# Kernel tuning notes

Hardware: AMD Instinct MI355X
Metric: run time of the kernel (lower is better)

Reference implementation:

```python
import jax, jax.numpy as jnp
import numpy as np

M = 100        # n_models
D = 16         # input_dim
H = 128        # hidden_dim
O = 1          # output_dim
NH = 4         # n_hidden
N = 16384      # batch of query points


def setup_inputs() -> dict:
    key = jax.random.key(0)
    ks = jax.random.split(key, 9)
    s = 0.1
    return {
        "x": jax.random.normal(ks[0], (N, D), dtype=jnp.float32),
        "W1": jax.random.normal(ks[1], (M, H, D), dtype=jnp.float32) * s,
        "b1": jax.random.normal(ks[2], (M, H), dtype=jnp.float32) * s,
        "Wh": jax.random.normal(ks[3], (M, NH, H, H), dtype=jnp.float32) * s,
        "bh": jax.random.normal(ks[4], (M, NH, H), dtype=jnp.float32) * s,
        "Wmu": jax.random.normal(ks[5], (M, O, H), dtype=jnp.float32) * s,
        "bmu": jax.random.normal(ks[6], (M, O), dtype=jnp.float32) * s,
        "Wsig": jax.random.normal(ks[7], (M, O, H), dtype=jnp.float32) * s,
        "bsig": jax.random.normal(ks[8], (M, O), dtype=jnp.float32) * s,
    }


def reference(x, W1, b1, Wh, bh, Wmu, bmu, Wsig, bsig):
    # Batched across all M models: h has shape [M, N, H]
    h = jax.nn.relu(jnp.einsum("nd,mhd->mnh", x, W1) + b1[:, None, :])
    for i in range(NH):  # fixed small structural loop over hidden layers
        h = jax.nn.relu(jnp.einsum("mnh,mkh->mnk", h, Wh[:, i]) + bh[:, i][:, None, :])
    mu = jnp.einsum("mnh,moh->mno", h, Wmu) + bmu[:, None, :]      # [M, N, O]
    sigma = jnp.exp(jnp.einsum("mnh,moh->mno", h, Wsig) + bsig[:, None, :])
    return (mu, sigma)
```

## Files before the change

kernel.cpp:

```cpp
#include <hip/hip_runtime.h>


typedef float  f32x4  __attribute__((ext_vector_type(4)));
typedef float  f32x16 __attribute__((ext_vector_type(16)));
typedef __bf16 bf16x4 __attribute__((ext_vector_type(4)));
typedef __bf16 bf16x8 __attribute__((ext_vector_type(8)));
typedef short  s16x4  __attribute__((ext_vector_type(4)));

union BF4  { bf16x4 v; uint2 u2; };
union FRAG { bf16x8 v; uint4 u4; };
union PKW  { uint2 u2; s16x4 s4; };

#define MODELS 100
#define NPT    16384
#define HDIM   128
#define SG_OFF (MODELS * NPT)

#define XB_OFF   0
#define W1B_OFF  262144
#define WHB_OFF  466944
#define WMU_OFF  7020544
#define WSG_OFF  7033344

#define GTOT 880768

__global__ __launch_bounds__(256) void cvt_weights(
    const float* __restrict__ x,   const float* __restrict__ W1,
    const float* __restrict__ Wh,  const float* __restrict__ Wmu,
    const float* __restrict__ Wsg, unsigned short* __restrict__ ws)
{
  int gid = blockIdx.x * 256 + threadIdx.x;
  if (gid >= GTOT) return;
  const float* src;
  unsigned int dst;
  if (gid < 32768) {
    src = x + gid * 8;                       dst = XB_OFF + gid * 8;
  } else if (gid < 58368) {
    int g = gid - 32768;
    src = W1 + g * 8;                        dst = W1B_OFF + g * 8;
  } else if (gid < 877568) {
    int g = gid - 58368;
    int chunk  = g >> 11;
    int within = g & 2047;
    int r   = within >> 4;
    int j   = within & 15;
    src = Wh + (size_t)g * 8;
    dst = WHB_OFF + chunk * 16384 + (j * 128 + r) * 8;
  } else if (gid < 879168) {
    int g = gid - 877568;
    src = Wmu + g * 8;                       dst = WMU_OFF + g * 8;
  } else {
    int g = gid - 879168;
    src = Wsg + g * 8;                       dst = WSG_OFF + g * 8;
  }
  f32x4 a = *(const f32x4*)src;
  f32x4 b = *(const f32x4*)(src + 4);
  BF4 lo, hi;
  lo.v = __builtin_convertvector(a, bf16x4);
  hi.v = __builtin_convertvector(b, bf16x4);
  uint4 u; u.x = lo.u2.x; u.y = lo.u2.y; u.z = hi.u2.x; u.w = hi.u2.y;
  *(uint4*)&ws[dst] = u;
}

__device__ __forceinline__ void gload_lds16(const void* g, void* l) {
  __builtin_amdgcn_global_load_lds(
      (const __attribute__((address_space(1))) void*)g,
      (__attribute__((address_space(3))) void*)l, 16, 0, 0);
}

#define MFMA32(A,B,C) __builtin_amdgcn_mfma_f32_32x32x16_bf16((A),(B),(C),0,0,0)

__device__ __forceinline__ void build_hfrag(const f32x16 (&acc)[2][4],
                                            uint4 (&hf)[2][8]) {
  const s16x4 z4 = {0, 0, 0, 0};
  #pragma unroll
  for (int nt = 0; nt < 2; ++nt) {
    #pragma unroll
    for (int kt2 = 0; kt2 < 4; ++kt2) {
      uint2 P[4];
      #pragma unroll
      for (int q = 0; q < 4; ++q) {
        f32x4 v;
        v[0] = acc[nt][kt2][4*q+0]; v[1] = acc[nt][kt2][4*q+1];
        v[2] = acc[nt][kt2][4*q+2]; v[3] = acc[nt][kt2][4*q+3];
        BF4 b; b.v = __builtin_convertvector(v, bf16x4);
        PKW p; p.u2 = b.u2;
        p.s4 = __builtin_elementwise_max(p.s4, z4);
        P[q] = p.u2;
      }
      #pragma unroll
      for (int sb = 0; sb < 2; ++sb) {
        unsigned int x0 = P[2*sb].x, y0 = P[2*sb+1].x;
        unsigned int x1 = P[2*sb].y, y1 = P[2*sb+1].y;
        asm("v_permlane32_swap_b32 %0, %1" : "+v"(x0), "+v"(y0));
        asm("v_permlane32_swap_b32 %0, %1" : "+v"(x1), "+v"(y1));
        uint4 f; f.x = x0; f.y = x1; f.z = y0; f.w = y1;
        hf[nt][2*kt2+sb] = f;
      }
    }
  }
}

__global__ __launch_bounds__(512, 2) void ens_mlp(
    const unsigned short* __restrict__ ws,
    const float* __restrict__ b1,  const float* __restrict__ bh,
    const float* __restrict__ bmu, const float* __restrict__ bsg,
    float* __restrict__ out)
{
  __shared__ unsigned short wlds[4 * HDIM * HDIM];

  const int bid = blockIdx.x;
  const int swz = (bid & 7) * 400 + (bid >> 3);
  const int m   = swz >> 5;
  const int nb0 = (swz & 31) << 9;

  const int t    = threadIdx.x;
  const int lane = t & 63;
  const int wv   = t >> 6;
  const int l31  = lane & 31;
  const int hi   = lane >> 5;
  const int nbw  = nb0 + wv * 64;

  {
    const char* src = (const char*)(ws + WHB_OFF + m * 65536);
    char* dst = (char*)wlds;
    #pragma unroll
    for (int it = 0; it < 16; ++it) {
      int off = t * 16 + it * 8192;
      gload_lds16(src + off, dst + off);
    }
  }

  uint4  hfrag[2][8];
  f32x16 acc[2][4];

  auto layer1 = [&]() {
    const unsigned short* W1m = ws + W1B_OFF + m * (HDIM * 16);
    const unsigned short* xp  = ws + XB_OFF;
    FRAG w1f[4], xf[2];
    #pragma unroll
    for (int kt2 = 0; kt2 < 4; ++kt2)
      w1f[kt2].v = *(const bf16x8*)&W1m[(kt2 * 32 + l31) * 16 + hi * 8];
    #pragma unroll
    for (int nt = 0; nt < 2; ++nt)
      xf[nt].v = *(const bf16x8*)&xp[(nbw + nt * 32 + l31) * 16 + hi * 8];
    #pragma unroll
    for (int kt2 = 0; kt2 < 4; ++kt2) {
      union { f32x16 v; f32x4 q[4]; } C;
      #pragma unroll
      for (int q = 0; q < 4; ++q)
        C.q[q] = *(const f32x4*)(b1 + m * HDIM + kt2 * 32 + q * 8 + hi * 4);
      #pragma unroll
      for (int nt = 0; nt < 2; ++nt)
        acc[nt][kt2] = MFMA32(w1f[kt2].v, xf[nt].v, C.v);
    }
    build_hfrag(acc, hfrag);
  };

  if (wv < 4) layer1();
  __syncthreads();
  if (wv >= 4) layer1();

  #pragma unroll
  for (int i = 0; i < 4; ++i) {
    const unsigned short* wl = wlds + i * 16384 + l31 * 8 + hi * 1024;
    const float* bp = bh + m * 512 + i * HDIM;

    union { f32x16 v; f32x4 q[4]; } C[4];
    #pragma unroll
    for (int kt2 = 0; kt2 < 4; ++kt2)
      #pragma unroll
      for (int q = 0; q < 4; ++q)
        C[kt2].q[q] = *(const f32x4*)(bp + kt2 * 32 + q * 8 + hi * 4);

    #pragma unroll
    for (int ks = 0; ks < 8; ++ks) {
      FRAG wf[4];
      #pragma unroll
      for (int kt2 = 0; kt2 < 4; ++kt2)
        wf[kt2].u4 = *(const uint4*)(wl + kt2 * 256 + ks * 2048);
      #pragma unroll
      for (int kt2 = 0; kt2 < 4; ++kt2)
        #pragma unroll
        for (int nt = 0; nt < 2; ++nt) {
          FRAG hv; hv.u4 = hfrag[nt][ks];
          acc[nt][kt2] = MFMA32(wf[kt2].v, hv.v,
                                ks == 0 ? C[kt2].v : acc[nt][kt2]);
        }
    }
    build_hfrag(acc, hfrag);
  }

  {
    FRAG hw[8];
    const unsigned short* wp = ws + (l31 == 0 ? WMU_OFF : WSG_OFF) + m * HDIM;
    #pragma unroll
    for (int ks = 0; ks < 8; ++ks) {
      if (l31 < 2) {
        hw[ks].v = *(const bf16x8*)&wp[ks * 16 + hi * 8];
      } else {
        uint4 z; z.x = 0u; z.y = 0u; z.z = 0u; z.w = 0u;
        hw[ks].u4 = z;
      }
    }
    f32x16 C;
    #pragma unroll
    for (int j = 0; j < 16; ++j) C[j] = 0.0f;
    if (hi == 0) { C[0] = bmu[m]; C[1] = bsg[m]; }

    #pragma unroll
    for (int nt = 0; nt < 2; ++nt) {
      f32x16 a2;
      #pragma unroll
      for (int ks = 0; ks < 8; ++ks) {
        FRAG hv; hv.u4 = hfrag[nt][ks];
        a2 = MFMA32(hw[ks].v, hv.v, ks == 0 ? C : a2);
      }
      if (hi == 0) {
        int n = nbw + nt * 32 + l31;
        out[m * NPT + n]          = a2[0];
        out[SG_OFF + m * NPT + n] = expf(a2[1]);
      }
    }
  }
}

extern "C" void kernel_launch(void* const* d_in, const int* in_sizes, int n_in,
                              void* d_out, int out_size, void* d_ws, size_t ws_size,
                              hipStream_t stream) {
  const float* x   = (const float*)d_in[0];
  const float* W1  = (const float*)d_in[1];
  const float* b1  = (const float*)d_in[2];
  const float* Wh  = (const float*)d_in[3];
  const float* bh  = (const float*)d_in[4];
  const float* Wmu = (const float*)d_in[5];
  const float* bmu = (const float*)d_in[6];
  const float* Wsg = (const float*)d_in[7];
  const float* bsg = (const float*)d_in[8];
  unsigned short* ws = (unsigned short*)d_ws;
  (void)in_sizes; (void)n_in; (void)out_size; (void)ws_size;

  cvt_weights<<<(GTOT + 255) / 256, 256, 0, stream>>>(x, W1, Wh, Wmu, Wsg, ws);
  ens_mlp<<<3200, 512, 0, stream>>>(ws, b1, bh, bmu, bsg, (float*)d_out);
}
```

Before: 225.1 us.

## Ping-pong two point tiles so activation conversion overlaps MFMA work

```diff
diff --git a/kernel.cpp b/kernel.cpp
--- a/kernel.cpp
+++ b/kernel.cpp
@@ -7,9 +7,7 @@
 typedef __bf16 bf16x8 __attribute__((ext_vector_type(8)));
 typedef short  s16x4  __attribute__((ext_vector_type(4)));
 
-union BF4  { bf16x4 v; uint2 u2; };
-union FRAG { bf16x8 v; uint4 u4; };
-union PKW  { uint2 u2; s16x4 s4; };
+union BF4 { bf16x4 v; uint2 u2; };
 
 #define MODELS 100
 #define NPT    16384
@@ -70,34 +68,27 @@
 
 #define MFMA32(A,B,C) __builtin_amdgcn_mfma_f32_32x32x16_bf16((A),(B),(C),0,0,0)
 
-__device__ __forceinline__ void build_hfrag(const f32x16 (&acc)[2][4],
-                                            uint4 (&hf)[2][8]) {
+__device__ __forceinline__ void build_chunk(const f32x16& a, bf16x8 (&hf)[8],
+                                            int base) {
   const s16x4 z4 = {0, 0, 0, 0};
-  #pragma unroll
-  for (int nt = 0; nt < 2; ++nt) {
-    #pragma unroll
-    for (int kt2 = 0; kt2 < 4; ++kt2) {
-      uint2 P[4];
-      #pragma unroll
-      for (int q = 0; q < 4; ++q) {
-        f32x4 v;
-        v[0] = acc[nt][kt2][4*q+0]; v[1] = acc[nt][kt2][4*q+1];
-        v[2] = acc[nt][kt2][4*q+2]; v[3] = acc[nt][kt2][4*q+3];
-        BF4 b; b.v = __builtin_convertvector(v, bf16x4);
-        PKW p; p.u2 = b.u2;
-        p.s4 = __builtin_elementwise_max(p.s4, z4);
-        P[q] = p.u2;
-      }
-      #pragma unroll
-      for (int sb = 0; sb < 2; ++sb) {
-        unsigned int x0 = P[2*sb].x, y0 = P[2*sb+1].x;
-        unsigned int x1 = P[2*sb].y, y1 = P[2*sb+1].y;
-        asm("v_permlane32_swap_b32 %0, %1" : "+v"(x0), "+v"(y0));
-        asm("v_permlane32_swap_b32 %0, %1" : "+v"(x1), "+v"(y1));
-        uint4 f; f.x = x0; f.y = x1; f.z = y0; f.w = y1;
-        hf[nt][2*kt2+sb] = f;
-      }
-    }
+  uint2 P[4];
+  #pragma unroll
+  for (int q = 0; q < 4; ++q) {
+    f32x4 v;
+    v[0] = a[4*q+0]; v[1] = a[4*q+1]; v[2] = a[4*q+2]; v[3] = a[4*q+3];
+    bf16x4 b = __builtin_convertvector(v, bf16x4);
+    s16x4 s = __builtin_bit_cast(s16x4, b);
+    s = __builtin_elementwise_max(s, z4);
+    P[q] = __builtin_bit_cast(uint2, s);
+  }
+  #pragma unroll
+  for (int sb = 0; sb < 2; ++sb) {
+    unsigned int x0 = P[2*sb].x, y0 = P[2*sb+1].x;
+    unsigned int x1 = P[2*sb].y, y1 = P[2*sb+1].y;
+    asm("v_permlane32_swap_b32 %0, %1" : "+v"(x0), "+v"(y0));
+    asm("v_permlane32_swap_b32 %0, %1" : "+v"(x1), "+v"(y1));
+    uint4 f; f.x = x0; f.y = x1; f.z = y0; f.w = y1;
+    hf[base + sb] = __builtin_bit_cast(bf16x8, f);
   }
 }
 
@@ -131,35 +122,33 @@
     }
   }
 
-  uint4  hfrag[2][8];
-  f32x16 acc[2][4];
-
-  auto layer1 = [&]() {
+  bf16x8 hf0[8], hf1[8];
+  f32x16 acc0[4], acc1[4];
+
+  {
     const unsigned short* W1m = ws + W1B_OFF + m * (HDIM * 16);
     const unsigned short* xp  = ws + XB_OFF;
-    FRAG w1f[4], xf[2];
+    bf16x8 w1f[4], xf0, xf1;
     #pragma unroll
     for (int kt2 = 0; kt2 < 4; ++kt2)
-      w1f[kt2].v = *(const bf16x8*)&W1m[(kt2 * 32 + l31) * 16 + hi * 8];
-    #pragma unroll
-    for (int nt = 0; nt < 2; ++nt)
-      xf[nt].v = *(const bf16x8*)&xp[(nbw + nt * 32 + l31) * 16 + hi * 8];
+      w1f[kt2] = *(const bf16x8*)&W1m[(kt2 * 32 + l31) * 16 + hi * 8];
+    xf0 = *(const bf16x8*)&xp[(nbw +      l31) * 16 + hi * 8];
+    xf1 = *(const bf16x8*)&xp[(nbw + 32 + l31) * 16 + hi * 8];
     #pragma unroll
     for (int kt2 = 0; kt2 < 4; ++kt2) {
       union { f32x16 v; f32x4 q[4]; } C;
       #pragma unroll
       for (int q = 0; q < 4; ++q)
         C.q[q] = *(const f32x4*)(b1 + m * HDIM + kt2 * 32 + q * 8 + hi * 4);
-      #pragma unroll
-      for (int nt = 0; nt < 2; ++nt)
-        acc[nt][kt2] = MFMA32(w1f[kt2].v, xf[nt].v, C.v);
-    }
-    build_hfrag(acc, hfrag);
-  };
-
-  if (wv < 4) layer1();
+      acc0[kt2] = MFMA32(w1f[kt2], xf0, C.v);
+      acc1[kt2] = MFMA32(w1f[kt2], xf1, C.v);
+    }
+  }
+  #pragma unroll
+  for (int kt2 = 0; kt2 < 4; ++kt2)
+    build_chunk(acc0[kt2], hf0, 2 * kt2);
+
   __syncthreads();
-  if (wv >= 4) layer1();
 
   #pragma unroll
   for (int i = 0; i < 4; ++i) {
@@ -175,32 +164,44 @@
 
     #pragma unroll
     for (int ks = 0; ks < 8; ++ks) {
-      FRAG wf[4];
-      #pragma unroll
-      for (int kt2 = 0; kt2 < 4; ++kt2)
-        wf[kt2].u4 = *(const uint4*)(wl + kt2 * 256 + ks * 2048);
-      #pragma unroll
-      for (int kt2 = 0; kt2 < 4; ++kt2)
-        #pragma unroll
-        for (int nt = 0; nt < 2; ++nt) {
-          FRAG hv; hv.u4 = hfrag[nt][ks];
-          acc[nt][kt2] = MFMA32(wf[kt2].v, hv.v,
-                                ks == 0 ? C[kt2].v : acc[nt][kt2]);
-        }
-    }
-    build_hfrag(acc, hfrag);
-  }
+      bf16x8 wf[4];
+      #pragma unroll
+      for (int kt2 = 0; kt2 < 4; ++kt2)
+        wf[kt2] = *(const bf16x8*)(wl + kt2 * 256 + ks * 2048);
+      #pragma unroll
+      for (int kt2 = 0; kt2 < 4; ++kt2)
+        acc0[kt2] = MFMA32(wf[kt2], hf0[ks], ks == 0 ? C[kt2].v : acc0[kt2]);
+      if (ks < 4)
+        build_chunk(acc1[ks], hf1, 2 * ks);
+    }
+
+    #pragma unroll
+    for (int ks = 0; ks < 8; ++ks) {
+      bf16x8 wf[4];
+      #pragma unroll
+      for (int kt2 = 0; kt2 < 4; ++kt2)
+        wf[kt2] = *(const bf16x8*)(wl + kt2 * 256 + ks * 2048);
+      #pragma unroll
+      for (int kt2 = 0; kt2 < 4; ++kt2)
+        acc1[kt2] = MFMA32(wf[kt2], hf1[ks], ks == 0 ? C[kt2].v : acc1[kt2]);
+      if (ks < 4)
+        build_chunk(acc0[ks], hf0, 2 * ks);
+    }
+  }
+  #pragma unroll
+  for (int kt2 = 0; kt2 < 4; ++kt2)
+    build_chunk(acc1[kt2], hf1, 2 * kt2);
 
   {
-    FRAG hw[8];
+    bf16x8 hw[8];
     const unsigned short* wp = ws + (l31 == 0 ? WMU_OFF : WSG_OFF) + m * HDIM;
     #pragma unroll
     for (int ks = 0; ks < 8; ++ks) {
       if (l31 < 2) {
-        hw[ks].v = *(const bf16x8*)&wp[ks * 16 + hi * 8];
+        hw[ks] = *(const bf16x8*)&wp[ks * 16 + hi * 8];
       } else {
         uint4 z; z.x = 0u; z.y = 0u; z.z = 0u; z.w = 0u;
-        hw[ks].u4 = z;
+        hw[ks] = __builtin_bit_cast(bf16x8, z);
       }
     }
     f32x16 C;
@@ -208,19 +209,22 @@
     for (int j = 0; j < 16; ++j) C[j] = 0.0f;
     if (hi == 0) { C[0] = bmu[m]; C[1] = bsg[m]; }
 
-    #pragma unroll
-    for (int nt = 0; nt < 2; ++nt) {
-      f32x16 a2;
-      #pragma unroll
-      for (int ks = 0; ks < 8; ++ks) {
-        FRAG hv; hv.u4 = hfrag[nt][ks];
-        a2 = MFMA32(hw[ks].v, hv.v, ks == 0 ? C : a2);
-      }
-      if (hi == 0) {
-        int n = nbw + nt * 32 + l31;
-        out[m * NPT + n]          = a2[0];
-        out[SG_OFF + m * NPT + n] = expf(a2[1]);
-      }
+    f32x16 a2;
+    #pragma unroll
+    for (int ks = 0; ks < 8; ++ks)
+      a2 = MFMA32(hw[ks], hf0[ks], ks == 0 ? C : a2);
+    if (hi == 0) {
+      int n = nbw + l31;
+      out[m * NPT + n]          = a2[0];
+      out[SG_OFF + m * NPT + n] = expf(a2[1]);
+    }
+    #pragma unroll
+    for (int ks = 0; ks < 8; ++ks)
+      a2 = MFMA32(hw[ks], hf1[ks], ks == 0 ? C : a2);
+    if (hi == 0) {
+      int n = nbw + 32 + l31;
+      out[m * NPT + n]          = a2[0];
+      out[SG_OFF + m * NPT + n] = expf(a2[1]);
     }
   }
 }
```

Measured after the change: 402.2 us. 1.79x slower.
